# Kernel tuning notes

Measured on AMD Instinct MI355X. Metric: run time of the kernel, lower is better.

The kernel has to match this reference:

```python
import jax, jax.numpy as jnp
import numpy as np
from jax import lax

B, CHI, CHO, H, W = 8, 128, 128, 64, 64
K = 3
KK = K * K


def setup_inputs() -> dict:
    key = jax.random.key(0)
    ks = jax.random.split(key, 7)
    x = jax.random.normal(ks[0], (B, CHI, H, W), jnp.float32)
    # small offset-conv weights so sampled offsets stay in a realistic few-pixel range
    off_w = jax.random.normal(ks[1], (3 * KK, CHI, K, K), jnp.float32) * 0.01
    off_b = jnp.zeros((3 * KK,), jnp.float32)
    w = jax.random.normal(ks[2], (CHO, CHI, K, K), jnp.float32) / np.sqrt(CHI * KK).astype(np.float32)
    b = jnp.zeros((CHO,), jnp.float32)
    gamma = jax.random.uniform(ks[3], (CHO,), jnp.float32)  # nn.init.uniform_ on BN weight
    beta = jnp.zeros((CHO,), jnp.float32)
    return {"x": x, "off_w": off_w, "off_b": off_b, "w": w, "b": b, "gamma": gamma, "beta": beta}


def _deform_conv(x, off_w, off_b, w, b):
    """DCNv2 modulated deformable conv, k=3, stride=1, pad=1, dil=1, 1 deform group."""
    B_, C, H_, W_ = x.shape
    # offset/mask branch: plain 3x3 conv -> 27 channels (2*9 offsets, 9 masks)
    om = lax.conv_general_dilated(x, off_w, (1, 1), ((1, 1), (1, 1)),
                                  dimension_numbers=("NCHW", "OIHW", "NCHW"))
    om = om + off_b[None, :, None, None]
    off = om[:, : 2 * KK].reshape(B_, KK, 2, H_, W_)  # [B,9,2,H,W]; ch 2k=y, 2k+1=x
    mask = jax.nn.sigmoid(om[:, 2 * KK:])             # [B,9,H,W]

    ky, kx = jnp.meshgrid(jnp.arange(K, dtype=jnp.float32),
                          jnp.arange(K, dtype=jnp.float32), indexing="ij")
    ky = ky.reshape(KK); kx = kx.reshape(KK)
    # sampling positions: p = p0 - pad + k*dil + offset
    py = off[:, :, 0] + (jnp.arange(H_, dtype=jnp.float32) - 1.0)[None, None, :, None] + ky[None, :, None, None]
    px = off[:, :, 1] + (jnp.arange(W_, dtype=jnp.float32) - 1.0)[None, None, None, :] + kx[None, :, None, None]

    y0 = jnp.floor(py); x0 = jnp.floor(px)
    ly = py - y0; lx = px - x0
    xf = x.reshape(B_, C, H_ * W_)

    def corner(yi, xi, wgt):
        valid = ((yi >= 0) & (yi <= H_ - 1) & (xi >= 0) & (xi <= W_ - 1)).astype(x.dtype)
        yc = jnp.clip(yi, 0, H_ - 1).astype(jnp.int32)
        xc = jnp.clip(xi, 0, W_ - 1).astype(jnp.int32)
        idx = (yc * W_ + xc).reshape(B_, KK * H_ * W_)
        g = jax.vmap(lambda xb, ib: xb[:, ib])(xf, idx).reshape(B_, C, KK, H_, W_)
        return g * (valid * wgt)[:, None]

    val = (corner(y0, x0, (1 - ly) * (1 - lx))
           + corner(y0, x0 + 1, (1 - ly) * lx)
           + corner(y0 + 1, x0, ly * (1 - lx))
           + corner(y0 + 1, x0 + 1, ly * lx))  # [B,C,9,H,W]
    val = val * mask[:, None]  # modulation
    out = jnp.einsum("bckhw,ock->bohw", val, w.reshape(w.shape[0], C, KK))
    return out + b[None, :, None, None]


def reference(x, off_w, off_b, w, b, gamma, beta):
    y = _deform_conv(x, off_w, off_b, w, b)
    # BatchNorm2d in training mode (batch statistics), eps=1e-5, then ReLU
    mean = y.mean(axis=(0, 2, 3))
    var = y.var(axis=(0, 2, 3))
    yn = (y - mean[None, :, None, None]) * lax.rsqrt(var[None, :, None, None] + 1e-5)
    return jax.nn.relu(yn * gamma[None, :, None, None] + beta[None, :, None, None])
```

## Files before the change

kernel.cpp:

```cpp
#include <hip/hip_runtime.h>
#include <hip/hip_bf16.h>
#include <math.h>

#define HH 64
#define WW 64
#define HW 4096
#define LDV 136

typedef __bf16 bf16x8 __attribute__((ext_vector_type(8)));
typedef float floatx4 __attribute__((ext_vector_type(4)));
typedef unsigned int uint4a __attribute__((ext_vector_type(4)));
typedef unsigned int uint2a __attribute__((ext_vector_type(2)));

#define WS_Y    0u
#define WS_PSQ  16777216u
#define WS_XTB  16778240u
#define WS_WTB  25166848u
#define WS_OWB  25461760u

static __device__ inline ushort f2bf(float f) {
  __hip_bfloat16 h = __float2bfloat16(f);
  return __builtin_bit_cast(ushort, h);
}
static __device__ inline float lo16(unsigned int u) { return __builtin_bit_cast(float, u << 16); }
static __device__ inline float hi16(unsigned int u) { return __builtin_bit_cast(float, u & 0xffff0000u); }

__global__ __launch_bounds__(256) void k_prep(const float* __restrict__ x,
                                              const float* __restrict__ w,
                                              const float* __restrict__ ow,
                                              ushort* __restrict__ xtb,
                                              ushort* __restrict__ wtb,
                                              ushort* __restrict__ owb,
                                              float* __restrict__ psq) {
  __shared__ float tile[32][33];
  int bid = blockIdx.x;
  if (bid < 4096) {
    int hw0 = (bid & 127) * 32;
    int c0 = ((bid >> 7) & 3) * 32;
    int b = bid >> 9;
    int col = threadIdx.x & 31, row = threadIdx.x >> 5;
    const float* xb = x + ((size_t)b * 128 + c0) * HW + hw0;
#pragma unroll
    for (int i = 0; i < 32; i += 8)
      tile[row + i][col] = xb[(size_t)(row + i) * HW + col];
    __syncthreads();
    int hw = threadIdx.x >> 3, cq = threadIdx.x & 7;
    ushort* xo = xtb + ((size_t)b * HW + hw0) * 128 + c0;
    unsigned int lo = (unsigned int)f2bf(tile[cq * 4 + 0][hw]) |
                      ((unsigned int)f2bf(tile[cq * 4 + 1][hw]) << 16);
    unsigned int hi = (unsigned int)f2bf(tile[cq * 4 + 2][hw]) |
                      ((unsigned int)f2bf(tile[cq * 4 + 3][hw]) << 16);
    uint2a v2 = (uint2a){lo, hi};
    *(uint2a*)(&xo[(size_t)hw * 128 + cq * 4]) = v2;
  } else if (bid < 4096 + 576) {
    int idx = (bid - 4096) * 256 + threadIdx.x;
    int c = idx & 127, o = (idx >> 7) & 127, k = idx >> 14;
    wtb[idx] = f2bf(w[(o * 128 + c) * 9 + k]);
  } else if (bid < 4096 + 720) {
    int j = (bid - 4672) * 256 + threadIdx.x;
    int c = j & 127, o = (j >> 7) & 31, k = j >> 12;
    float v = (o < 27) ? ow[(o * 128 + c) * 9 + k] : 0.f;
    owb[j] = f2bf(v);
  } else {
    psq[threadIdx.x] = 0.f;
  }
}

__global__ __launch_bounds__(256) void k_main(
    const ushort* __restrict__ xtb, const ushort* __restrict__ wtb,
    const ushort* __restrict__ owb, const float* __restrict__ off_b,
    const float* __restrict__ bias, float* __restrict__ y) {
  __shared__ ushort Vl[2][32 * LDV];
  __shared__ float omL[27 * 32];
  int t = threadIdx.x;
  int lane = t & 63, wv = t >> 6;
  int li = lane & 15, quad = lane >> 4;
  int hr = blockIdx.x;
  int row = hr >> 1, p0b = (hr & 1) * 32;
  int b = blockIdx.y;
  const ushort* xb = xtb + (size_t)b * HW * 128;
  int ch = t & 15;
  int pq = t >> 4;

  int mi = wv & 1, ni = wv >> 1;
  floatx4 oacc = (floatx4){0.f, 0.f, 0.f, 0.f};
  uint4a u0, u1;
  auto p1load = [&](int k, int p, uint4a& u) {
    int ky = k / 3, kx = k % 3;
    int ry = row - 1 + ky, cx = p0b + p - 1 + kx;
    bool v = (ry >= 0 && ry < HH && cx >= 0 && cx < WW);
    int idx = v ? (ry * WW + cx) : 0;
    uint4a a = *(const uint4a*)(xb + (size_t)idx * 128 + ch * 8);
    u = v ? a : (uint4a){0u, 0u, 0u, 0u};
  };
  p1load(0, pq, u0);
  p1load(0, pq + 16, u1);
  for (int k = 0; k < 9; ++k) {
    *(uint4a*)(&Vl[k & 1][pq * LDV + ch * 8]) = u0;
    *(uint4a*)(&Vl[k & 1][(pq + 16) * LDV + ch * 8]) = u1;
    if (k < 8) {
      p1load(k + 1, pq, u0);
      p1load(k + 1, pq + 16, u1);
    }
    __syncthreads();
#pragma unroll
    for (int ks = 0; ks < 4; ++ks) {
      bf16x8 bfrag = __builtin_bit_cast(bf16x8,
          *(const uint4a*)(&Vl[k & 1][(ni * 16 + li) * LDV + ks * 32 + quad * 8]));
      bf16x8 afrag = __builtin_bit_cast(bf16x8,
          *(const uint4a*)(&owb[(size_t)(k * 32 + mi * 16 + li) * 128 + ks * 32 + quad * 8]));
      oacc = __builtin_amdgcn_mfma_f32_16x16x32_bf16(afrag, bfrag, oacc, 0, 0, 0);
    }
  }
#pragma unroll
  for (int r = 0; r < 4; ++r) {
    int o = mi * 16 + quad * 4 + r;
    if (o < 27) omL[o * 32 + ni * 16 + li] = oacc[r] + off_b[o];
  }
  __syncthreads();

  floatx4 macc[2][2];
#pragma unroll
  for (int i = 0; i < 2; ++i)
#pragma unroll
    for (int j = 0; j < 2; ++j) macc[i][j] = (floatx4){0.f, 0.f, 0.f, 0.f};

  float wqA[4], wqB[4];
  int idxA[4], idxB[4];
  uint4a u[8];

  auto prep = [&](int k, int p, float* wq, int* idx4) {
    int ky = k / 3, kx = k % 3;
    float offy = omL[(2 * k) * 32 + p];
    float offx = omL[(2 * k + 1) * 32 + p];
    float mraw = omL[(18 + k) * 32 + p];
    float m = 1.f / (1.f + __expf(-mraw));
    float py = offy + (float)(row - 1 + ky);
    float px = offx + (float)(p0b + p - 1 + kx);
    float y0f = floorf(py), x0f = floorf(px);
    float ly = py - y0f, lx = px - x0f;
    int iy0 = (int)y0f, ix0 = (int)x0f;
    int iy1 = iy0 + 1, ix1 = ix0 + 1;
    float w00 = (1.f - ly) * (1.f - lx) * m, w01 = (1.f - ly) * lx * m;
    float w10 = ly * (1.f - lx) * m, w11 = ly * lx * m;
    if (iy0 < 0 || iy0 > HH - 1) { w00 = 0.f; w01 = 0.f; }
    if (iy1 < 0 || iy1 > HH - 1) { w10 = 0.f; w11 = 0.f; }
    if (ix0 < 0 || ix0 > WW - 1) { w00 = 0.f; w10 = 0.f; }
    if (ix1 < 0 || ix1 > WW - 1) { w01 = 0.f; w11 = 0.f; }
    int cy0 = min(max(iy0, 0), HH - 1), cy1 = min(max(iy1, 0), HH - 1);
    int cx0 = min(max(ix0, 0), WW - 1), cx1 = min(max(ix1, 0), WW - 1);
    idx4[0] = cy0 * WW + cx0;
    idx4[1] = cy0 * WW + cx1;
    idx4[2] = cy1 * WW + cx0;
    idx4[3] = cy1 * WW + cx1;
    wq[0] = w00; wq[1] = w01; wq[2] = w10; wq[3] = w11;
  };
  auto issue = [&]() {
#pragma unroll
    for (int c = 0; c < 4; ++c)
      u[c] = *(const uint4a*)(xb + (size_t)idxA[c] * 128 + ch * 8);
#pragma unroll
    for (int c = 0; c < 4; ++c)
      u[4 + c] = *(const uint4a*)(xb + (size_t)idxB[c] * 128 + ch * 8);
  };

  prep(0, pq, wqA, idxA);
  prep(0, pq + 16, wqB, idxB);
  issue();
  for (int k = 0; k < 9; ++k) {
    {
      uint4a outv;
#pragma unroll
      for (int e = 0; e < 4; ++e) {
        float rlo = wqA[0] * lo16(u[0][e]) + wqA[1] * lo16(u[1][e]) +
                    wqA[2] * lo16(u[2][e]) + wqA[3] * lo16(u[3][e]);
        float rhi = wqA[0] * hi16(u[0][e]) + wqA[1] * hi16(u[1][e]) +
                    wqA[2] * hi16(u[2][e]) + wqA[3] * hi16(u[3][e]);
        outv[e] = (unsigned int)f2bf(rlo) | ((unsigned int)f2bf(rhi) << 16);
      }
      *(uint4a*)(&Vl[k & 1][pq * LDV + ch * 8]) = outv;
    }
    {
      uint4a outv;
#pragma unroll
      for (int e = 0; e < 4; ++e) {
        float rlo = wqB[0] * lo16(u[4][e]) + wqB[1] * lo16(u[5][e]) +
                    wqB[2] * lo16(u[6][e]) + wqB[3] * lo16(u[7][e]);
        float rhi = wqB[0] * hi16(u[4][e]) + wqB[1] * hi16(u[5][e]) +
                    wqB[2] * hi16(u[6][e]) + wqB[3] * hi16(u[7][e]);
        outv[e] = (unsigned int)f2bf(rlo) | ((unsigned int)f2bf(rhi) << 16);
      }
      *(uint4a*)(&Vl[k & 1][(pq + 16) * LDV + ch * 8]) = outv;
    }
    if (k < 8) {
      prep(k + 1, pq, wqA, idxA);
      prep(k + 1, pq + 16, wqB, idxB);
      issue();
    }
    __syncthreads();
    const ushort* Arow = &wtb[(size_t)(k * 128 + wv * 32) * 128];
#pragma unroll
    for (int ks = 0; ks < 4; ++ks) {
      bf16x8 b0 = __builtin_bit_cast(bf16x8,
          *(const uint4a*)(&Vl[k & 1][(li)*LDV + ks * 32 + quad * 8]));
      bf16x8 b1 = __builtin_bit_cast(bf16x8,
          *(const uint4a*)(&Vl[k & 1][(16 + li) * LDV + ks * 32 + quad * 8]));
      bf16x8 a0 = __builtin_bit_cast(bf16x8,
          *(const uint4a*)(Arow + (size_t)(li)*128 + ks * 32 + quad * 8));
      bf16x8 a1 = __builtin_bit_cast(bf16x8,
          *(const uint4a*)(Arow + (size_t)(16 + li) * 128 + ks * 32 + quad * 8));
      macc[0][0] = __builtin_amdgcn_mfma_f32_16x16x32_bf16(a0, b0, macc[0][0], 0, 0, 0);
      macc[0][1] = __builtin_amdgcn_mfma_f32_16x16x32_bf16(a0, b1, macc[0][1], 0, 0, 0);
      macc[1][0] = __builtin_amdgcn_mfma_f32_16x16x32_bf16(a1, b0, macc[1][0], 0, 0, 0);
      macc[1][1] = __builtin_amdgcn_mfma_f32_16x16x32_bf16(a1, b1, macc[1][1], 0, 0, 0);
    }
  }
#pragma unroll
  for (int ot = 0; ot < 2; ++ot)
#pragma unroll
    for (int pt = 0; pt < 2; ++pt)
#pragma unroll
      for (int r = 0; r < 4; ++r) {
        int o = wv * 32 + ot * 16 + quad * 4 + r;
        int p = p0b + pt * 16 + li;
        y[((size_t)(b * 128 + o)) * HW + row * 64 + p] = macc[ot][pt][r] + bias[o];
      }
}

__global__ __launch_bounds__(256) void k_stats(const float* __restrict__ y,
                                               float* __restrict__ psq) {
  int o = blockIdx.x, b = blockIdx.y, t = threadIdx.x;
  const float4* yb = (const float4*)(y + ((size_t)(b * 128 + o)) * HW);
  float s = 0.f, q = 0.f;
#pragma unroll
  for (int i = 0; i < 4; ++i) {
    float4 v = yb[t + i * 256];
    s += v.x + v.y + v.z + v.w;
    q += v.x * v.x + v.y * v.y + v.z * v.z + v.w * v.w;
  }
#pragma unroll
  for (int off = 32; off >= 1; off >>= 1) {
    s += __shfl_down(s, off, 64);
    q += __shfl_down(q, off, 64);
  }
  __shared__ float bs[4], bq[4];
  if ((t & 63) == 0) { bs[t >> 6] = s; bq[t >> 6] = q; }
  __syncthreads();
  if (t == 0) {
    atomicAdd(&psq[o], bs[0] + bs[1] + bs[2] + bs[3]);
    atomicAdd(&psq[128 + o], bq[0] + bq[1] + bq[2] + bq[3]);
  }
}

__global__ __launch_bounds__(256) void k_norm(const float* __restrict__ y,
                                              const float* __restrict__ psq,
                                              const float* __restrict__ gamma,
                                              const float* __restrict__ beta,
                                              float* __restrict__ out) {
  int blk = blockIdx.x;
  int o = (blk >> 2) & 127;
  float s = psq[o], q = psq[128 + o];
  float mean = s * (1.f / 32768.f);
  float var = q * (1.f / 32768.f) - mean * mean;
  float scale = gamma[o] * rsqrtf(var + 1e-5f);
  float shift = beta[o] - mean * scale;
  int i4 = blk * 256 + threadIdx.x;
  float4 v = ((const float4*)y)[i4];
  float4 r;
  r.x = fmaxf(v.x * scale + shift, 0.f);
  r.y = fmaxf(v.y * scale + shift, 0.f);
  r.z = fmaxf(v.z * scale + shift, 0.f);
  r.w = fmaxf(v.w * scale + shift, 0.f);
  ((float4*)out)[i4] = r;
}

extern "C" void kernel_launch(void* const* d_in, const int* in_sizes, int n_in,
                              void* d_out, int out_size, void* d_ws, size_t ws_size,
                              hipStream_t stream) {
  const float* x     = (const float*)d_in[0];
  const float* off_w = (const float*)d_in[1];
  const float* off_b = (const float*)d_in[2];
  const float* w     = (const float*)d_in[3];
  const float* bias  = (const float*)d_in[4];
  const float* gamma = (const float*)d_in[5];
  const float* beta  = (const float*)d_in[6];
  float* out = (float*)d_out;
  char* ws = (char*)d_ws;

  float* y    = (float*)(ws + WS_Y);
  float* psq  = (float*)(ws + WS_PSQ);
  ushort* xtb = (ushort*)(ws + WS_XTB);
  ushort* wtb = (ushort*)(ws + WS_WTB);
  ushort* owb = (ushort*)(ws + WS_OWB);

  k_prep<<<4817, 256, 0, stream>>>(x, w, off_w, xtb, wtb, owb, psq);
  k_main<<<dim3(128, 8), 256, 0, stream>>>(xtb, wtb, owb, off_b, bias, y);
  k_stats<<<dim3(128, 8), 256, 0, stream>>>(y, psq);
  k_norm<<<4096, 256, 0, stream>>>(y, psq, gamma, beta, out);
}
```

Before: 155.3 us.

## Feed bilinear samples straight into MFMA registers with split-K across waves

Each wave now gathers and interpolates its own 32-channel slice of the sampled values directly in the MFMA B-fragment register layout. This removes the LDS staging buffer and the per-tap __syncthreads in the main loop. In exchange, each wave accumulates all 128 output channels as partial sums over its channel slice (16 accumulator tiles). Those partials are reduced across the four waves through LDS at the end, which adds more registers, extra weight loads per wave, and a serialized 8-step reduction with barriers.

New measurement: 193.6 us. +24.6%, slower.

```diff
diff --git a/kernel.cpp b/kernel.cpp
--- a/kernel.cpp
+++ b/kernel.cpp
@@ -70,7 +70,7 @@
     const ushort* __restrict__ xtb, const ushort* __restrict__ wtb,
     const ushort* __restrict__ owb, const float* __restrict__ off_b,
     const float* __restrict__ bias, float* __restrict__ y) {
-  __shared__ ushort Vl[2][32 * LDV];
+  __shared__ alignas(16) ushort Vl[2][32 * LDV];
   __shared__ float omL[27 * 32];
   int t = threadIdx.x;
   int lane = t & 63, wv = t >> 6;
@@ -119,11 +119,12 @@
   }
   __syncthreads();
 
-  floatx4 macc[2][2];
-#pragma unroll
-  for (int i = 0; i < 2; ++i)
-#pragma unroll
-    for (int j = 0; j < 2; ++j) macc[i][j] = (floatx4){0.f, 0.f, 0.f, 0.f};
+  floatx4 macc[8][2];
+#pragma unroll
+  for (int g = 0; g < 8; ++g) {
+    macc[g][0] = (floatx4){0.f, 0.f, 0.f, 0.f};
+    macc[g][1] = (floatx4){0.f, 0.f, 0.f, 0.f};
+  }
 
   float wqA[4], wqB[4];
   int idxA[4], idxB[4];
@@ -158,73 +159,82 @@
   auto issue = [&]() {
 #pragma unroll
     for (int c = 0; c < 4; ++c)
-      u[c] = *(const uint4a*)(xb + (size_t)idxA[c] * 128 + ch * 8);
+      u[c] = *(const uint4a*)(xb + (size_t)idxA[c] * 128 + wv * 32 + quad * 8);
 #pragma unroll
     for (int c = 0; c < 4; ++c)
-      u[4 + c] = *(const uint4a*)(xb + (size_t)idxB[c] * 128 + ch * 8);
+      u[4 + c] = *(const uint4a*)(xb + (size_t)idxB[c] * 128 + wv * 32 + quad * 8);
   };
 
-  prep(0, pq, wqA, idxA);
-  prep(0, pq + 16, wqB, idxB);
+  prep(0, li, wqA, idxA);
+  prep(0, 16 + li, wqB, idxB);
   issue();
   for (int k = 0; k < 9; ++k) {
-    {
-      uint4a outv;
-#pragma unroll
-      for (int e = 0; e < 4; ++e) {
-        float rlo = wqA[0] * lo16(u[0][e]) + wqA[1] * lo16(u[1][e]) +
-                    wqA[2] * lo16(u[2][e]) + wqA[3] * lo16(u[3][e]);
-        float rhi = wqA[0] * hi16(u[0][e]) + wqA[1] * hi16(u[1][e]) +
-                    wqA[2] * hi16(u[2][e]) + wqA[3] * hi16(u[3][e]);
-        outv[e] = (unsigned int)f2bf(rlo) | ((unsigned int)f2bf(rhi) << 16);
+    uint4a bv0, bv1;
+#pragma unroll
+    for (int e = 0; e < 4; ++e) {
+      float rlo = wqA[0] * lo16(u[0][e]) + wqA[1] * lo16(u[1][e]) +
+                  wqA[2] * lo16(u[2][e]) + wqA[3] * lo16(u[3][e]);
+      float rhi = wqA[0] * hi16(u[0][e]) + wqA[1] * hi16(u[1][e]) +
+                  wqA[2] * hi16(u[2][e]) + wqA[3] * hi16(u[3][e]);
+      bv0[e] = (unsigned int)f2bf(rlo) | ((unsigned int)f2bf(rhi) << 16);
+      float slo = wqB[0] * lo16(u[4][e]) + wqB[1] * lo16(u[5][e]) +
+                  wqB[2] * lo16(u[6][e]) + wqB[3] * lo16(u[7][e]);
+      float shi = wqB[0] * hi16(u[4][e]) + wqB[1] * hi16(u[5][e]) +
+                  wqB[2] * hi16(u[6][e]) + wqB[3] * hi16(u[7][e]);
+      bv1[e] = (unsigned int)f2bf(slo) | ((unsigned int)f2bf(shi) << 16);
+    }
+    bf16x8 b0 = __builtin_bit_cast(bf16x8, bv0);
+    bf16x8 b1 = __builtin_bit_cast(bf16x8, bv1);
+    if (k < 8) {
+      prep(k + 1, li, wqA, idxA);
+      prep(k + 1, 16 + li, wqB, idxB);
+      issue();
+    }
+    const ushort* Arow = wtb + (size_t)k * 128 * 128 + wv * 32 + quad * 8;
+#pragma unroll
+    for (int g = 0; g < 8; ++g) {
+      bf16x8 a = __builtin_bit_cast(bf16x8,
+          *(const uint4a*)(Arow + (size_t)(g * 16 + li) * 128));
+      macc[g][0] = __builtin_amdgcn_mfma_f32_16x16x32_bf16(a, b0, macc[g][0], 0, 0, 0);
+      macc[g][1] = __builtin_amdgcn_mfma_f32_16x16x32_bf16(a, b1, macc[g][1], 0, 0, 0);
+    }
+  }
+
+  float (*red)[8] = (float(*)[8])(&Vl[0][0]);
+  for (int g = 0; g < 8; ++g) {
+    int ow = g & 3;
+    __syncthreads();
+    if (wv != ow) {
+      int slot = wv - (wv > ow ? 1 : 0);
+#pragma unroll
+      for (int pt = 0; pt < 2; ++pt)
+#pragma unroll
+        for (int r = 0; r < 4; ++r)
+          red[slot * 64 + lane][pt * 4 + r] = macc[g][pt][r];
+    }
+    __syncthreads();
+    if (wv == ow) {
+#pragma unroll
+      for (int slot = 0; slot < 3; ++slot)
+#pragma unroll
+        for (int pt = 0; pt < 2; ++pt)
+#pragma unroll
+          for (int r = 0; r < 4; ++r)
+            macc[g][pt][r] += red[slot * 64 + lane][pt * 4 + r];
+    }
+  }
+#pragma unroll
+  for (int gg = 0; gg < 2; ++gg) {
+    int g = wv + gg * 4;
+#pragma unroll
+    for (int pt = 0; pt < 2; ++pt)
+#pragma unroll
+      for (int r = 0; r < 4; ++r) {
+        int o = g * 16 + quad * 4 + r;
+        int p = p0b + pt * 16 + li;
+        y[((size_t)(b * 128 + o)) * HW + row * 64 + p] = macc[g][pt][r] + bias[o];
       }
-      *(uint4a*)(&Vl[k & 1][pq * LDV + ch * 8]) = outv;
-    }
-    {
-      uint4a outv;
-#pragma unroll
-      for (int e = 0; e < 4; ++e) {
-        float rlo = wqB[0] * lo16(u[4][e]) + wqB[1] * lo16(u[5][e]) +
-                    wqB[2] * lo16(u[6][e]) + wqB[3] * lo16(u[7][e]);
-        float rhi = wqB[0] * hi16(u[4][e]) + wqB[1] * hi16(u[5][e]) +
-                    wqB[2] * hi16(u[6][e]) + wqB[3] * hi16(u[7][e]);
-        outv[e] = (unsigned int)f2bf(rlo) | ((unsigned int)f2bf(rhi) << 16);
-      }
-      *(uint4a*)(&Vl[k & 1][(pq + 16) * LDV + ch * 8]) = outv;
-    }
-    if (k < 8) {
-      prep(k + 1, pq, wqA, idxA);
-      prep(k + 1, pq + 16, wqB, idxB);
-      issue();
-    }
-    __syncthreads();
-    const ushort* Arow = &wtb[(size_t)(k * 128 + wv * 32) * 128];
-#pragma unroll
-    for (int ks = 0; ks < 4; ++ks) {
-      bf16x8 b0 = __builtin_bit_cast(bf16x8,
-          *(const uint4a*)(&Vl[k & 1][(li)*LDV + ks * 32 + quad * 8]));
-      bf16x8 b1 = __builtin_bit_cast(bf16x8,
-          *(const uint4a*)(&Vl[k & 1][(16 + li) * LDV + ks * 32 + quad * 8]));
-      bf16x8 a0 = __builtin_bit_cast(bf16x8,
-          *(const uint4a*)(Arow + (size_t)(li)*128 + ks * 32 + quad * 8));
-      bf16x8 a1 = __builtin_bit_cast(bf16x8,
-          *(const uint4a*)(Arow + (size_t)(16 + li) * 128 + ks * 32 + quad * 8));
-      macc[0][0] = __builtin_amdgcn_mfma_f32_16x16x32_bf16(a0, b0, macc[0][0], 0, 0, 0);
-      macc[0][1] = __builtin_amdgcn_mfma_f32_16x16x32_bf16(a0, b1, macc[0][1], 0, 0, 0);
-      macc[1][0] = __builtin_amdgcn_mfma_f32_16x16x32_bf16(a1, b0, macc[1][0], 0, 0, 0);
-      macc[1][1] = __builtin_amdgcn_mfma_f32_16x16x32_bf16(a1, b1, macc[1][1], 0, 0, 0);
-    }
-  }
-#pragma unroll
-  for (int ot = 0; ot < 2; ++ot)
-#pragma unroll
-    for (int pt = 0; pt < 2; ++pt)
-#pragma unroll
-      for (int r = 0; r < 4; ++r) {
-        int o = wv * 32 + ot * 16 + quad * 4 + r;
-        int p = p0b + pt * 16 + li;
-        y[((size_t)(b * 128 + o)) * HW + row * 64 + p] = macc[ot][pt][r] + bias[o];
-      }
+  }
 }
 
 __global__ __launch_bounds__(256) void k_stats(const float* __restrict__ y,
```
